# Kernel tuning notes

Hardware: AMD Instinct MI355X
Metric: run time of the kernel (lower is better)

The kernel has to match this reference:

```python
import jax, jax.numpy as jnp
import numpy as np
import math

L, N, D = 1024, 64, 64
O = 1024

def setup_inputs() -> dict:
    key = jax.random.key(0)
    k1, k2 = jax.random.split(key)
    x = jax.random.normal(k1, (L, N, D), dtype=jnp.float32)
    upfold = jax.random.normal(k2, (O, N, D), dtype=jnp.float32)
    return {"x": x, "upfold": upfold}

def reference(x, upfold):
    # x: [L, N, D], upfold: [O, N, D]
    d = x.shape[-1]
    scale = 1.0 / math.sqrt(d)
    # affinities: [L, O, N]
    affinities = jnp.einsum('lnd,ond->lon', x, upfold) * scale
    # weighted sum with (sigmoid - 0.5) weights: [L, N, D]
    features = jnp.einsum('lon,ond->lnd', jax.nn.sigmoid(affinities) - 0.5, upfold)
    return features
```

## Files before the change

### kernel.cpp

```cpp
#include <hip/hip_runtime.h>
#include <stdint.h>

#define L_DIM 1024
#define N_DIM 64
#define D_DIM 64
#define O_DIM 1024
#define ND    4096
#define UPAD  72
#define NT    8

typedef float    floatx16 __attribute__((ext_vector_type(16)));
typedef _Float16 half8    __attribute__((ext_vector_type(8)));
typedef _Float16 h2       __attribute__((ext_vector_type(2)));
typedef __fp16   fp16x2   __attribute__((ext_vector_type(2)));

__device__ __forceinline__ uint32_t pkh2(float a, float b) {
    fp16x2 p = __builtin_amdgcn_cvt_pkrtz(a, b);
    return __builtin_bit_cast(uint32_t, p);
}

__device__ __forceinline__ half8 mk_frag(uint32_t a, uint32_t b, uint32_t c, uint32_t d) {
    union { uint32_t u[4]; half8 v; } U;
    U.u[0] = a; U.u[1] = b; U.u[2] = c; U.u[3] = d;
    return U.v;
}

__device__ __forceinline__ uint32_t psig(float s0, float s1) {
    const h2 HI = {(_Float16)41.6f,        (_Float16)41.6f};
    const h2 LO = {(_Float16)-41.6f,       (_Float16)-41.6f};
    const h2 SC = {(_Float16)0.0625f,      (_Float16)0.0625f};
    const h2 C0 = {(_Float16)0.03099238f,  (_Float16)0.03099238f};
    const h2 C1 = {(_Float16)-0.00842090f, (_Float16)-0.00842090f};
    const h2 C2 = {(_Float16)0.00151845f,  (_Float16)0.00151845f};
    const h2 C3 = {(_Float16)-1.02197e-4f, (_Float16)-1.02197e-4f};
    h2 s = __builtin_bit_cast(h2, pkh2(s0, s1));
    s = __builtin_elementwise_min(s, HI);
    s = __builtin_elementwise_max(s, LO);
    h2 ha = s * SC;
    h2 v  = ha * ha;
    h2 w  = C2 + v * C3;
    w     = C1 + v * w;
    w     = C0 + v * w;
    h2 f  = s * w;
    return __builtin_bit_cast(uint32_t, f);
}

__global__ void __launch_bounds__(256, 4)
corr_kernel(const float* __restrict__ x, const float* __restrict__ up,
            float* __restrict__ out)
{
    __shared__ __align__(16) unsigned char smem[36864];
    uint16_t (*Ub)[64][UPAD] = (uint16_t (*)[64][UPAD])smem;
    uint16_t (*Ut)[64][UPAD] = (uint16_t (*)[64][UPAD])(smem + 18432);
    float    (*Fred)[2][2][32][16] = (float (*)[2][2][32][16])smem;

    const int tid  = threadIdx.x;
    const int lane = tid & 63;
    const int wid  = tid >> 6;
    const int l31  = lane & 31;
    const int h    = lane >> 5;
    const int team = wid >> 1;
    const int wrow = wid & 1;
    const int ttid = tid & 127;
    const int rp   = ttid & 31;
    const int cq   = ttid >> 5;
    const int n    = blockIdx.y;
    const int lw   = blockIdx.x * 64 + wrow * 32 + l31;

    const float* ubase = up + (size_t)n * D_DIM;

    half8 Xf[4];
    {
        const float* xp = x + (size_t)lw * ND + n * D_DIM + 8 * h;
        #pragma unroll
        for (int kk = 0; kk < 4; ++kk) {
            const float* p = xp + 16 * kk;
            Xf[kk] = mk_frag(pkh2(p[0], p[1]), pkh2(p[2], p[3]),
                             pkh2(p[4], p[5]), pkh2(p[6], p[7]));
        }
    }

    floatx16 F0, F1;
    #pragma unroll
    for (int i = 0; i < 16; ++i) { F0[i] = 0.0f; F1[i] = 0.0f; }

    float va[16], vb[16];
    {
        const float* pr = ubase + (size_t)(team * 512 + 2 * rp) * ND + 16 * cq;
        #pragma unroll
        for (int j = 0; j < 4; ++j) {
            float4 f = *(const float4*)(pr + 4 * j);
            va[4*j] = f.x; va[4*j+1] = f.y; va[4*j+2] = f.z; va[4*j+3] = f.w;
            float4 g = *(const float4*)(pr + ND + 4 * j);
            vb[4*j] = g.x; vb[4*j+1] = g.y; vb[4*j+2] = g.z; vb[4*j+3] = g.w;
        }
    }

    for (int ot = 0; ot < NT; ++ot) {
        *(uint4*)&Ub[team][2*rp][16*cq] =
            make_uint4(pkh2(va[0],va[1]),  pkh2(va[2],va[3]),
                       pkh2(va[4],va[5]),  pkh2(va[6],va[7]));
        *(uint4*)&Ub[team][2*rp][16*cq + 8] =
            make_uint4(pkh2(va[8],va[9]),  pkh2(va[10],va[11]),
                       pkh2(va[12],va[13]),pkh2(va[14],va[15]));
        *(uint4*)&Ub[team][2*rp+1][16*cq] =
            make_uint4(pkh2(vb[0],vb[1]),  pkh2(vb[2],vb[3]),
                       pkh2(vb[4],vb[5]),  pkh2(vb[6],vb[7]));
        *(uint4*)&Ub[team][2*rp+1][16*cq + 8] =
            make_uint4(pkh2(vb[8],vb[9]),  pkh2(vb[10],vb[11]),
                       pkh2(vb[12],vb[13]),pkh2(vb[14],vb[15]));
        #pragma unroll
        for (int j = 0; j < 16; ++j)
            *(uint32_t*)&Ut[team][16*cq + j][2*rp] = pkh2(va[j], vb[j]);
        __syncthreads();

        if (ot + 1 < NT) {
            const float* pr = ubase + (size_t)(team * 512 + (ot+1) * 64 + 2 * rp) * ND + 16 * cq;
            #pragma unroll
            for (int j = 0; j < 4; ++j) {
                float4 f = *(const float4*)(pr + 4 * j);
                va[4*j] = f.x; va[4*j+1] = f.y; va[4*j+2] = f.z; va[4*j+3] = f.w;
                float4 g = *(const float4*)(pr + ND + 4 * j);
                vb[4*j] = g.x; vb[4*j+1] = g.y; vb[4*j+2] = g.z; vb[4*j+3] = g.w;
            }
        }

        floatx16 S0, S1;
        #pragma unroll
        for (int i = 0; i < 16; ++i) { S0[i] = 0.0f; S1[i] = 0.0f; }
        #pragma unroll
        for (int kk = 0; kk < 4; ++kk) {
            half8 A0 = *(const half8*)&Ub[team][l31][16 * kk + 8 * h];
            half8 A1 = *(const half8*)&Ub[team][32 + l31][16 * kk + 8 * h];
            S0 = __builtin_amdgcn_mfma_f32_32x32x16_f16(A0, Xf[kk], S0, 0, 0, 0);
            S1 = __builtin_amdgcn_mfma_f32_32x32x16_f16(A1, Xf[kk], S1, 0, 0, 0);
        }

        uint32_t P[16];
        #pragma unroll
        for (int m = 0; m < 8; ++m) P[m]     = psig(S0[2*m], S0[2*m+1]);
        #pragma unroll
        for (int m = 0; m < 8; ++m) P[8 + m] = psig(S1[2*m], S1[2*m+1]);

        #pragma unroll
        for (int c = 0; c < 4; ++c) {
            const uint32_t* Q = P + (c >> 1) * 8;
            const int t4 = (c & 1) * 4;
            uint32_t s0 = h ? Q[t4]     : Q[t4 + 2];
            uint32_t s1 = h ? Q[t4 + 1] : Q[t4 + 3];
            uint32_t r0 = __shfl_xor(s0, 32);
            uint32_t r1 = __shfl_xor(s1, 32);
            half8 B = h ? mk_frag(r0, r1, Q[t4 + 2], Q[t4 + 3])
                        : mk_frag(Q[t4], Q[t4 + 1], r0, r1);
            half8 A0 = *(const half8*)&Ut[team][l31][16 * c + 8 * h];
            half8 A1 = *(const half8*)&Ut[team][32 + l31][16 * c + 8 * h];
            F0 = __builtin_amdgcn_mfma_f32_32x32x16_f16(A0, B, F0, 0, 0, 0);
            F1 = __builtin_amdgcn_mfma_f32_32x32x16_f16(A1, B, F1, 0, 0, 0);
        }
        __syncthreads();
    }

    {
        float* dst = &Fred[team][wrow][h][l31][0];
        const floatx16& Fexp = team ? F0 : F1;
        #pragma unroll
        for (int q = 0; q < 4; ++q)
            *(float4*)(dst + 4*q) = make_float4(Fexp[4*q], Fexp[4*q+1], Fexp[4*q+2], Fexp[4*q+3]);
    }
    __syncthreads();

    float* op = out + (size_t)lw * ND + n * D_DIM;
    if (team == 0) {
        const float* src = &Fred[1][wrow][h][l31][0];
        #pragma unroll
        for (int q = 0; q < 4; ++q) {
            float4 r = *(const float4*)(src + 4*q);
            float4 a; a.x = F0[4*q]   + r.x; a.y = F0[4*q+1] + r.y;
                      a.z = F0[4*q+2] + r.z; a.w = F0[4*q+3] + r.w;
            *(float4*)(op + 8*q + 4*h) = a;
        }
    } else {
        const float* src = &Fred[0][wrow][h][l31][0];
        #pragma unroll
        for (int q = 0; q < 4; ++q) {
            float4 r = *(const float4*)(src + 4*q);
            float4 a; a.x = F1[4*q]   + r.x; a.y = F1[4*q+1] + r.y;
                      a.z = F1[4*q+2] + r.z; a.w = F1[4*q+3] + r.w;
            *(float4*)(op + 32 + 8*q + 4*h) = a;
        }
    }
}

extern "C" void kernel_launch(void* const* d_in, const int* in_sizes, int n_in,
                              void* d_out, int out_size, void* d_ws, size_t ws_size,
                              hipStream_t stream)
{
    const float* x  = (const float*)d_in[0];
    const float* up = (const float*)d_in[1];
    float* out      = (float*)d_out;
    dim3 grid(L_DIM / 64, N_DIM);
    corr_kernel<<<grid, dim3(256), 0, stream>>>(x, up, out);
}
```

Before: 121.0 us.

## Double-buffer upfold tile prefetch, stage x through LDS, and swap grid order

Upfold tiles are now prefetched two iterations ahead into double-buffered register arrays, and the tile loop is fully unrolled so the buffer index is static. This is meant to hide more global load latency, at the cost of more registers, and launch bounds are relaxed from 4 to 3 waves to make room. The x fragment is now loaded coalesced into LDS with float4 reads and then re-read per lane, instead of scattered per-lane global loads. The grid axes are swapped so consecutive blocks share the same n and its upfold slice, which is meant to improve L2 reuse. All shuffles are issued before the MFMAs to overlap cross-lane latency.

```diff
diff --git a/kernel.cpp b/kernel.cpp
--- a/kernel.cpp
+++ b/kernel.cpp
@@ -45,7 +45,19 @@
     return __builtin_bit_cast(uint32_t, f);
 }
 
-__global__ void __launch_bounds__(256, 4)
+__device__ __forceinline__ void load_tile(const float* ubase, int team, int ot,
+                                          int rp, int cq, float* va, float* vb) {
+    const float* pr = ubase + (size_t)(team * 512 + ot * 64 + 2 * rp) * ND + 16 * cq;
+    #pragma unroll
+    for (int j = 0; j < 4; ++j) {
+        float4 f = *(const float4*)(pr + 4 * j);
+        va[4*j] = f.x; va[4*j+1] = f.y; va[4*j+2] = f.z; va[4*j+3] = f.w;
+        float4 g = *(const float4*)(pr + ND + 4 * j);
+        vb[4*j] = g.x; vb[4*j+1] = g.y; vb[4*j+2] = g.z; vb[4*j+3] = g.w;
+    }
+}
+
+__global__ void __launch_bounds__(256, 3)
 corr_kernel(const float* __restrict__ x, const float* __restrict__ up,
             float* __restrict__ out)
 {
@@ -53,6 +65,7 @@
     uint16_t (*Ub)[64][UPAD] = (uint16_t (*)[64][UPAD])smem;
     uint16_t (*Ut)[64][UPAD] = (uint16_t (*)[64][UPAD])(smem + 18432);
     float    (*Fred)[2][2][32][16] = (float (*)[2][2][32][16])smem;
+    float    (*Xs)[68] = (float (*)[68])smem;
 
     const int tid  = threadIdx.x;
     const int lane = tid & 63;
@@ -64,66 +77,64 @@
     const int ttid = tid & 127;
     const int rp   = ttid & 31;
     const int cq   = ttid >> 5;
-    const int n    = blockIdx.y;
-    const int lw   = blockIdx.x * 64 + wrow * 32 + l31;
+    const int n    = blockIdx.x;
+    const int lb   = blockIdx.y;
+    const int lw   = lb * 64 + wrow * 32 + l31;
 
     const float* ubase = up + (size_t)n * D_DIM;
+
+    float va[2][16], vb[2][16];
+    load_tile(ubase, team, 0, rp, cq, va[0], vb[0]);
+    load_tile(ubase, team, 1, rp, cq, va[1], vb[1]);
 
     half8 Xf[4];
     {
-        const float* xp = x + (size_t)lw * ND + n * D_DIM + 8 * h;
+        const int xr = tid >> 2;
+        const int xc = tid & 3;
+        const float* xsrc = x + (size_t)(lb * 64 + xr) * ND + n * D_DIM;
+        #pragma unroll
+        for (int j = 0; j < 4; ++j) {
+            float4 f = *(const float4*)(xsrc + 4 * (xc + 4 * j));
+            *(float4*)&Xs[xr][4 * (xc + 4 * j)] = f;
+        }
+        __syncthreads();
+        const int rl = wrow * 32 + l31;
         #pragma unroll
         for (int kk = 0; kk < 4; ++kk) {
-            const float* p = xp + 16 * kk;
-            Xf[kk] = mk_frag(pkh2(p[0], p[1]), pkh2(p[2], p[3]),
-                             pkh2(p[4], p[5]), pkh2(p[6], p[7]));
-        }
+            float4 f1 = *(const float4*)&Xs[rl][16 * kk + 8 * h];
+            float4 f2 = *(const float4*)&Xs[rl][16 * kk + 8 * h + 4];
+            Xf[kk] = mk_frag(pkh2(f1.x, f1.y), pkh2(f1.z, f1.w),
+                             pkh2(f2.x, f2.y), pkh2(f2.z, f2.w));
+        }
+        __syncthreads();
     }
 
     floatx16 F0, F1;
     #pragma unroll
     for (int i = 0; i < 16; ++i) { F0[i] = 0.0f; F1[i] = 0.0f; }
 
-    float va[16], vb[16];
-    {
-        const float* pr = ubase + (size_t)(team * 512 + 2 * rp) * ND + 16 * cq;
-        #pragma unroll
-        for (int j = 0; j < 4; ++j) {
-            float4 f = *(const float4*)(pr + 4 * j);
-            va[4*j] = f.x; va[4*j+1] = f.y; va[4*j+2] = f.z; va[4*j+3] = f.w;
-            float4 g = *(const float4*)(pr + ND + 4 * j);
-            vb[4*j] = g.x; vb[4*j+1] = g.y; vb[4*j+2] = g.z; vb[4*j+3] = g.w;
-        }
-    }
-
+    #pragma unroll
     for (int ot = 0; ot < NT; ++ot) {
+        const int b = ot & 1;
         *(uint4*)&Ub[team][2*rp][16*cq] =
-            make_uint4(pkh2(va[0],va[1]),  pkh2(va[2],va[3]),
-                       pkh2(va[4],va[5]),  pkh2(va[6],va[7]));
+            make_uint4(pkh2(va[b][0],va[b][1]),  pkh2(va[b][2],va[b][3]),
+                       pkh2(va[b][4],va[b][5]),  pkh2(va[b][6],va[b][7]));
         *(uint4*)&Ub[team][2*rp][16*cq + 8] =
-            make_uint4(pkh2(va[8],va[9]),  pkh2(va[10],va[11]),
-                       pkh2(va[12],va[13]),pkh2(va[14],va[15]));
+            make_uint4(pkh2(va[b][8],va[b][9]),  pkh2(va[b][10],va[b][11]),
+                       pkh2(va[b][12],va[b][13]),pkh2(va[b][14],va[b][15]));
         *(uint4*)&Ub[team][2*rp+1][16*cq] =
-            make_uint4(pkh2(vb[0],vb[1]),  pkh2(vb[2],vb[3]),
-                       pkh2(vb[4],vb[5]),  pkh2(vb[6],vb[7]));
+            make_uint4(pkh2(vb[b][0],vb[b][1]),  pkh2(vb[b][2],vb[b][3]),
+                       pkh2(vb[b][4],vb[b][5]),  pkh2(vb[b][6],vb[b][7]));
         *(uint4*)&Ub[team][2*rp+1][16*cq + 8] =
-            make_uint4(pkh2(vb[8],vb[9]),  pkh2(vb[10],vb[11]),
-                       pkh2(vb[12],vb[13]),pkh2(vb[14],vb[15]));
+            make_uint4(pkh2(vb[b][8],vb[b][9]),  pkh2(vb[b][10],vb[b][11]),
+                       pkh2(vb[b][12],vb[b][13]),pkh2(vb[b][14],vb[b][15]));
         #pragma unroll
         for (int j = 0; j < 16; ++j)
-            *(uint32_t*)&Ut[team][16*cq + j][2*rp] = pkh2(va[j], vb[j]);
-        __syncthreads();
-
-        if (ot + 1 < NT) {
-            const float* pr = ubase + (size_t)(team * 512 + (ot+1) * 64 + 2 * rp) * ND + 16 * cq;
-            #pragma unroll
-            for (int j = 0; j < 4; ++j) {
-                float4 f = *(const float4*)(pr + 4 * j);
-                va[4*j] = f.x; va[4*j+1] = f.y; va[4*j+2] = f.z; va[4*j+3] = f.w;
-                float4 g = *(const float4*)(pr + ND + 4 * j);
-                vb[4*j] = g.x; vb[4*j+1] = g.y; vb[4*j+2] = g.z; vb[4*j+3] = g.w;
-            }
-        }
+            *(uint32_t*)&Ut[team][16*cq + j][2*rp] = pkh2(va[b][j], vb[b][j]);
+        __syncthreads();
+
+        if (ot + 2 < NT)
+            load_tile(ubase, team, ot + 2, rp, cq, va[b], vb[b]);
 
         floatx16 S0, S1;
         #pragma unroll
@@ -142,16 +153,20 @@
         #pragma unroll
         for (int m = 0; m < 8; ++m) P[8 + m] = psig(S1[2*m], S1[2*m+1]);
 
+        uint32_t R[8];
         #pragma unroll
         for (int c = 0; c < 4; ++c) {
             const uint32_t* Q = P + (c >> 1) * 8;
             const int t4 = (c & 1) * 4;
-            uint32_t s0 = h ? Q[t4]     : Q[t4 + 2];
-            uint32_t s1 = h ? Q[t4 + 1] : Q[t4 + 3];
-            uint32_t r0 = __shfl_xor(s0, 32);
-            uint32_t r1 = __shfl_xor(s1, 32);
-            half8 B = h ? mk_frag(r0, r1, Q[t4 + 2], Q[t4 + 3])
-                        : mk_frag(Q[t4], Q[t4 + 1], r0, r1);
+            R[2*c]   = __shfl_xor(h ? Q[t4]     : Q[t4 + 2], 32);
+            R[2*c+1] = __shfl_xor(h ? Q[t4 + 1] : Q[t4 + 3], 32);
+        }
+        #pragma unroll
+        for (int c = 0; c < 4; ++c) {
+            const uint32_t* Q = P + (c >> 1) * 8;
+            const int t4 = (c & 1) * 4;
+            half8 B = h ? mk_frag(R[2*c], R[2*c+1], Q[t4 + 2], Q[t4 + 3])
+                        : mk_frag(Q[t4], Q[t4 + 1], R[2*c], R[2*c+1]);
             half8 A0 = *(const half8*)&Ut[team][l31][16 * c + 8 * h];
             half8 A1 = *(const half8*)&Ut[team][32 + l31][16 * c + 8 * h];
             F0 = __builtin_amdgcn_mfma_f32_32x32x16_f16(A0, B, F0, 0, 0, 0);
@@ -198,6 +213,6 @@
     const float* x  = (const float*)d_in[0];
     const float* up = (const float*)d_in[1];
     float* out      = (float*)d_out;
-    dim3 grid(L_DIM / 64, N_DIM);
+    dim3 grid(N_DIM, L_DIM / 64);
     corr_kernel<<<grid, dim3(256), 0, stream>>>(x, up, out);
 }
```

After: 135.3 us. 1.12x slower.
